# Kernel optimization log

Hardware: AMD Instinct MI355X
Metric: run time of the kernel (lower is better)

The kernel has to match this reference:

```python
import jax, jax.numpy as jnp
import numpy as np

# Production-scale graph dims (see shape_source)
N = 50000      # nodes
E = 800000     # edges (avg degree 16)
C_IN = 128     # input feature dim
H = 96         # hidden (per species: prey X and predator Y)
C_OUT = 40     # num_classes
L = 5          # LVConv layers
DT = 0.05      # integration step


def setup_inputs() -> dict:
    key = jax.random.key(0)
    ks = jax.random.split(key, 14)
    x = jax.random.normal(ks[0], (N, C_IN), jnp.float32)
    edge_index = jax.random.randint(ks[1], (2, E), 0, N, dtype=jnp.int32)
    # lift linears
    Wx = jax.random.normal(ks[2], (C_IN, H), jnp.float32) / np.sqrt(C_IN)
    bx = jnp.zeros((H,), jnp.float32)
    Wy = jax.random.normal(ks[3], (C_IN, H), jnp.float32) / np.sqrt(C_IN)
    by = jnp.zeros((H,), jnp.float32)
    # per-layer Lotka-Volterra coefficients (per-channel), small positive scale
    alpha = 0.1 * jax.random.uniform(ks[4], (L, H), jnp.float32)
    beta  = 0.1 * jax.random.uniform(ks[5], (L, H), jnp.float32)
    gamma = 0.1 * jax.random.uniform(ks[6], (L, H), jnp.float32)
    delta = 0.1 * jax.random.uniform(ks[7], (L, H), jnp.float32)
    # readout on concat([X, Y])
    Wr = jax.random.normal(ks[8], (2 * H, C_OUT), jnp.float32) / np.sqrt(2 * H)
    br = jnp.zeros((C_OUT,), jnp.float32)
    return {"x": x, "edge_index": edge_index, "Wx": Wx, "bx": bx,
            "Wy": Wy, "by": by, "alpha": alpha, "beta": beta,
            "gamma": gamma, "delta": delta, "Wr": Wr, "br": br}


def reference(x, edge_index, Wx, bx, Wy, by, alpha, beta, gamma, delta, Wr, br):
    src, dst = edge_index[0], edge_index[1]
    # in-degree for mean aggregation over incoming edges
    deg = jax.ops.segment_sum(jnp.ones((E,), x.dtype), dst, num_segments=N)
    deg_inv = (1.0 / jnp.maximum(deg, 1.0))[:, None]  # [N,1]

    def mean_agg(v):  # [N,H] -> [N,H] neighbor mean (src -> dst)
        return jax.ops.segment_sum(v[src], dst, num_segments=N) * deg_inv

    # lift to prey (X) and predator (Y) populations
    X = jnp.tanh(x @ Wx + bx)
    Y = jnp.tanh(x @ Wy + by)
    # dropout is identity in eval mode (training=False)
    for l in range(L):
        aggX = mean_agg(X)
        aggY = mean_agg(Y)
        # explicit-Euler Lotka-Volterra dynamics on the graph
        Xn = X + DT * X * (alpha[l] - beta[l] * aggY)
        Yn = Y + DT * Y * (-gamma[l] + delta[l] * aggX)
        X, Y = Xn, Yn
    h = jnp.concatenate([X, Y], axis=-1)  # [N, 2H]
    return h @ Wr + br
```

## Files before the change

### kernel.cpp

```cpp
#include <hip/hip_runtime.h>
#include <hip/hip_bf16.h>
#include <hip/hip_fp16.h>


#define HDIM 96
#define CIN 128
#define COUT 40
#define NLAYER 5
#define DTC 0.05f

#define BK_SHIFT 7
#define BK_SIZE 128
#define EPB 2048
#define BCAP 3072
#define BSTRIDE 4096

typedef float  vfloat2 __attribute__((ext_vector_type(2)));
typedef float  vfloat4 __attribute__((ext_vector_type(4)));
typedef short  vshort8 __attribute__((ext_vector_type(8)));

__device__ __forceinline__ unsigned bf16_rne(float f) {
    unsigned u = __float_as_uint(f);
    return (u + 0x7fffu + ((u >> 16) & 1u)) >> 16;
}

__device__ __forceinline__ unsigned pack_bf16_pair(float xf, float yf) {
    return bf16_rne(xf) | (bf16_rne(yf) << 16);
}

__device__ __forceinline__ unsigned pack_f16_pair(float a, float b) {
    unsigned ha = (unsigned)__half_as_ushort(__float2half_rn(a));
    unsigned hb = (unsigned)__half_as_ushort(__float2half_rn(b));
    return ha | (hb << 16);
}

__device__ __forceinline__ float f16_lo(unsigned u) {
    return __half2float(__ushort_as_half((unsigned short)(u & 0xffffu)));
}
__device__ __forceinline__ float f16_hi(unsigned u) {
    return __half2float(__ushort_as_half((unsigned short)(u >> 16)));
}

__device__ __forceinline__ unsigned pack_fp8_quad(float x0, float y0, float x1, float y1) {
    int lo = __builtin_amdgcn_cvt_pk_fp8_f32(x0, y0, 0, false);
    int full = __builtin_amdgcn_cvt_pk_fp8_f32(x1, y1, lo, true);
    return (unsigned)full;
}

__device__ __forceinline__ float fast_tanh(float x) {
    float e = __expf(2.0f * x);
    return 1.0f - 2.0f * __builtin_amdgcn_rcpf(e + 1.0f);
}


__global__ __launch_bounds__(256) void wprep_kernel(
    const float* __restrict__ Wx, const float* __restrict__ bx,
    const float* __restrict__ Wy, const float* __restrict__ by,
    unsigned short* __restrict__ WcT, float* __restrict__ bc,
    int* __restrict__ gcur, int NB,
    unsigned* __restrict__ F0, unsigned* __restrict__ F1, int N) {
    int t = blockIdx.x * blockDim.x + threadIdx.x;
    if (t < NB) gcur[t] = 0;
    if (t < 192 * 128) {
        int cc = t >> 7;
        int k = t & 127;
        int h = cc >> 1;
        float w = (cc & 1) ? Wy[k * HDIM + h] : Wx[k * HDIM + h];
        WcT[cc * 128 + k] = (unsigned short)bf16_rne(w);
    }
    if (t < 192) {
        int h = t >> 1;
        bc[t] = (t & 1) ? by[h] : bx[h];
    }
    if (blockIdx.x == 0 && threadIdx.x < 48) {
        int plane = threadIdx.x >> 4, d = threadIdx.x & 15;
        size_t o = ((size_t)plane * (N + 1) + N) * 16 + d;
        F0[o] = 0u;
        F1[o] = 0u;
    }
}


__global__ __launch_bounds__(256) void bscatter_kernel(
    const int* __restrict__ src, const int* __restrict__ dst,
    int* __restrict__ gcur, unsigned* __restrict__ packed, int E, int NB) {
    __shared__ int h[512];
    __shared__ int cur[512];
    for (int i = threadIdx.x; i < NB; i += 256) h[i] = 0;
    __syncthreads();
    int base = blockIdx.x * EPB;
    int end = min(E, base + EPB);
    for (int e = base + threadIdx.x; e < end; e += 256)
        atomicAdd(&h[dst[e] >> BK_SHIFT], 1);
    __syncthreads();
    for (int i = threadIdx.x; i < NB; i += 256)
        cur[i] = h[i] ? atomicAdd(&gcur[i], h[i]) : 0;
    __syncthreads();
    for (int e = base + threadIdx.x; e < end; e += 256) {
        int d = dst[e];
        int b = d >> BK_SHIFT;
        int pos = atomicAdd(&cur[b], 1);
        if (pos < BCAP)
            packed[(size_t)b * BCAP + pos] =
                (unsigned)src[e] | ((unsigned)(d & (BK_SIZE - 1)) << 17);
    }
}


__global__ __launch_bounds__(256) void bcsr_kernel(
    const unsigned* __restrict__ packed, const int* __restrict__ gcur,
    uint2* __restrict__ rowinfo, unsigned short* __restrict__ csr, int N, int NB) {
    __shared__ int ldeg[BK_SIZE];
    __shared__ int sscan[BK_SIZE];
    __shared__ int lcur[BK_SIZE];
    int b = blockIdx.x;
    int t = threadIdx.x;
    int cnt = min(gcur[b], BCAP);
    const unsigned* pk = packed + (size_t)b * BCAP;
    int wbase = b * BSTRIDE;
    if (t < BK_SIZE) ldeg[t] = 0;
    __syncthreads();
    for (int e = t; e < cnt; e += 256)
        atomicAdd(&ldeg[(pk[e] >> 17) & (BK_SIZE - 1)], 1);
    __syncthreads();
    int deg = 0, pad = 0;
    if (t < BK_SIZE) {
        deg = ldeg[t];
        pad = (deg + 7) & ~7;
        sscan[t] = pad;
    }
    __syncthreads();
    for (int off = 1; off < BK_SIZE; off <<= 1) {
        int tv = (t < BK_SIZE && t >= off) ? sscan[t - off] : 0;
        __syncthreads();
        if (t < BK_SIZE) sscan[t] += tv;
        __syncthreads();
    }
    int gpos = 0;
    if (t < BK_SIZE) {
        gpos = wbase + sscan[t] - pad;
        lcur[t] = gpos;
        int node = b * BK_SIZE + t;
        if (node < N) {
            rowinfo[node] = make_uint2(
                (unsigned)gpos | ((unsigned)(pad >> 2) << 21),
                __float_as_uint(1.0f / fmaxf((float)deg, 1.0f)));
        }
    }
    __syncthreads();
    for (int e = t; e < cnt; e += 256) {
        unsigned p = pk[e];
        int l = (p >> 17) & (BK_SIZE - 1);
        int pos = atomicAdd(&lcur[l], 1);
        csr[pos] = (unsigned short)(p & 0x1FFFFu);
    }
    __syncthreads();
    if (t < BK_SIZE) {
        for (int p = lcur[t]; p < gpos + pad; p++) csr[p] = (unsigned short)N;
    }
}


#define LW_STRIDE 136
#define TILE_STRIDE 200

__global__ __launch_bounds__(256) void lift_mfma_kernel(
    const float* __restrict__ x, const unsigned short* __restrict__ WcT,
    const float* __restrict__ bc, unsigned* __restrict__ S,
    unsigned* __restrict__ F, int N) {
    __shared__ __align__(16) char smem[192 * LW_STRIDE * 2];
    __shared__ float sBc[192];
    unsigned short* sW = (unsigned short*)smem;
    unsigned short* tile = (unsigned short*)smem;
    int t = threadIdx.x;

    {
        const unsigned* g = (const unsigned*)WcT;
        unsigned* s = (unsigned*)sW;
        for (int i = t; i < 192 * 64; i += 256) {
            int cc = i >> 6;
            int kp = i & 63;
            s[cc * (LW_STRIDE / 2) + kp] = g[i];
        }
    }
    if (t < 192) sBc[t] = bc[t];
    __syncthreads();

    int wv = t >> 6;
    int lane = t & 63;
    int quad = lane >> 4;
    int m = lane & 15;
    int mbase = blockIdx.x * 64 + wv * 16;

    int anode = mbase + m;
    if (anode >= N) anode = N - 1;
    const float* xrow = x + (size_t)anode * CIN;

    vfloat4 acc[12];
#pragma unroll
    for (int i = 0; i < 12; i++) acc[i] = (vfloat4){0.f, 0.f, 0.f, 0.f};

#pragma unroll
    for (int kt = 0; kt < 4; kt++) {
        int k0 = kt * 32 + quad * 8;
        float4 xa = *(const float4*)(xrow + k0);
        float4 xb = *(const float4*)(xrow + k0 + 4);
        uint4 ua;
        ua.x = pack_bf16_pair(xa.x, xa.y);
        ua.y = pack_bf16_pair(xa.z, xa.w);
        ua.z = pack_bf16_pair(xb.x, xb.y);
        ua.w = pack_bf16_pair(xb.z, xb.w);
        vshort8 a = *(vshort8*)&ua;
#pragma unroll
        for (int nt = 0; nt < 12; nt++) {
            vshort8 b = *(const vshort8*)&sW[(nt * 16 + m) * LW_STRIDE + k0];
            acc[nt] = __builtin_amdgcn_mfma_f32_16x16x32_bf16(a, b, acc[nt], 0, 0, 0);
        }
    }

    __syncthreads();
#pragma unroll
    for (int nt = 0; nt < 12; nt++) {
        int ccb = nt * 16 + m;
        float bco = sBc[ccb];
#pragma unroll
        for (int r = 0; r < 4; r++) {
            int nl = wv * 16 + quad * 4 + r;
            float v = fast_tanh(acc[nt][r] + bco);
            tile[nl * TILE_STRIDE + ccb] = __half_as_ushort(__float2half_rn(v));
        }
    }
    __syncthreads();

    int nbase = blockIdx.x * 64;
#pragma unroll
    for (int i = 0; i < 6; i++) {
        int idx = i * 256 + t;
        int nl = idx / 24;
        int pos = idx - nl * 24;
        int node = nbase + nl;
        uint4 u = *(const uint4*)&tile[nl * TILE_STRIDE + pos * 8];
        if (node < N) {
            *(uint4*)(S + (size_t)node * 96 + pos * 4) = u;
            float f0 = f16_lo(u.x), f1 = f16_hi(u.x);
            float f2 = f16_lo(u.y), f3 = f16_hi(u.y);
            float f4 = f16_lo(u.z), f5 = f16_hi(u.z);
            float f6 = f16_lo(u.w), f7 = f16_hi(u.w);
            uint2 fq = make_uint2(pack_fp8_quad(f0, f1, f2, f3),
                                  pack_fp8_quad(f4, f5, f6, f7));
            int plane = pos >> 3;
            int slot = (2 * pos) & 15;
            *(uint2*)(F + ((size_t)plane * (N + 1) + node) * 16 + slot) = fq;
        }
    }
}


__global__ __launch_bounds__(256) void layer_kernel(
    const unsigned* __restrict__ F, unsigned* __restrict__ S,
    unsigned* __restrict__ Fn,
    const uint2* __restrict__ rowinfo, const unsigned short* __restrict__ csr,
    const float* __restrict__ alpha, const float* __restrict__ beta,
    const float* __restrict__ gamma, const float* __restrict__ delta,
    int N, int nblk) {
    int bid = blockIdx.x;
    int plane = bid / nblk;
    int tile = bid - plane * nblk;
    unsigned pstride = (unsigned)(N + 1) * 16u;
    const unsigned* Fp = F + (size_t)plane * pstride;

    int wave = threadIdx.x >> 6;
    int lane = threadIdx.x & 63;
    int li = lane & 7;
    unsigned tli = (unsigned)(2 * li);

    int node = tile * 32 + wave * 8 + (lane >> 3);
    bool nvalid = node < N;
    int nclamp = nvalid ? node : N - 1;
    uint2 ri = rowinfo[nclamp];
    unsigned beg = ri.x & 0x1FFFFFu;
    int cnt = nvalid ? (int)((ri.x >> 21) << 2) : 0;
    float dinv = __uint_as_float(ri.y);

    vfloat2 a0 = {0.f, 0.f}, a1 = {0.f, 0.f}, a2 = {0.f, 0.f}, a3 = {0.f, 0.f};

#define UNP(u)                                                              \
    do {                                                                    \
        a0 += __builtin_amdgcn_cvt_pk_f32_fp8((int)(u).x, false);           \
        a1 += __builtin_amdgcn_cvt_pk_f32_fp8((int)(u).x, true);            \
        a2 += __builtin_amdgcn_cvt_pk_f32_fp8((int)(u).y, false);           \
        a3 += __builtin_amdgcn_cvt_pk_f32_fp8((int)(u).y, true);            \
    } while (0)

    for (int j = 0; j < cnt; j += 8) {
        uint4 w = *(const uint4*)(csr + beg + (unsigned)j);
        unsigned o0 = ((w.x & 0xffffu) << 4) + tli;
        unsigned o1 = ((w.x >> 16) << 4) + tli;
        unsigned o2 = ((w.y & 0xffffu) << 4) + tli;
        unsigned o3 = ((w.y >> 16) << 4) + tli;
        unsigned o4 = ((w.z & 0xffffu) << 4) + tli;
        unsigned o5 = ((w.z >> 16) << 4) + tli;
        unsigned o6 = ((w.w & 0xffffu) << 4) + tli;
        unsigned o7 = ((w.w >> 16) << 4) + tli;
        uint2 u0 = *(const uint2*)(Fp + o0);
        uint2 u1 = *(const uint2*)(Fp + o1);
        uint2 u2 = *(const uint2*)(Fp + o2);
        uint2 u3 = *(const uint2*)(Fp + o3);
        uint2 u4 = *(const uint2*)(Fp + o4);
        uint2 u5 = *(const uint2*)(Fp + o5);
        uint2 u6 = *(const uint2*)(Fp + o6);
        uint2 u7 = *(const uint2*)(Fp + o7);
        UNP(u0); UNP(u1); UNP(u2); UNP(u3);
        UNP(u4); UNP(u5); UNP(u6); UNP(u7);
    }
#undef UNP

    if (!nvalid) return;

    int h0 = plane * 32 + 4 * li;
    float4 av = *(const float4*)(alpha + h0);
    float4 bv = *(const float4*)(beta + h0);
    float4 gv = *(const float4*)(gamma + h0);
    float4 dv = *(const float4*)(delta + h0);
    unsigned* srow = S + (size_t)node * 96 + h0;
    uint4 su = *(const uint4*)srow;

    float x0 = f16_lo(su.x), y0 = f16_hi(su.x);
    float x1 = f16_lo(su.y), y1 = f16_hi(su.y);
    float x2 = f16_lo(su.z), y2 = f16_hi(su.z);
    float x3 = f16_lo(su.w), y3 = f16_hi(su.w);

    float ox0 = x0 + DTC * x0 * (av.x - bv.x * (a0.y * dinv));
    float oy0 = y0 + DTC * y0 * (-gv.x + dv.x * (a0.x * dinv));
    float ox1 = x1 + DTC * x1 * (av.y - bv.y * (a1.y * dinv));
    float oy1 = y1 + DTC * y1 * (-gv.y + dv.y * (a1.x * dinv));
    float ox2 = x2 + DTC * x2 * (av.z - bv.z * (a2.y * dinv));
    float oy2 = y2 + DTC * y2 * (-gv.z + dv.z * (a2.x * dinv));
    float ox3 = x3 + DTC * x3 * (av.w - bv.w * (a3.y * dinv));
    float oy3 = y3 + DTC * y3 * (-gv.w + dv.w * (a3.x * dinv));

    uint4 so;
    so.x = pack_f16_pair(ox0, oy0);
    so.y = pack_f16_pair(ox1, oy1);
    so.z = pack_f16_pair(ox2, oy2);
    so.w = pack_f16_pair(ox3, oy3);
    *(uint4*)srow = so;

    if (Fn) {
        uint2 fo;
        fo.x = pack_fp8_quad(ox0, oy0, ox1, oy1);
        fo.y = pack_fp8_quad(ox2, oy2, ox3, oy3);
        *(uint2*)(Fn + (size_t)plane * pstride + (unsigned)node * 16u + tli) = fo;
    }
}


#define WG_STRIDE 200

__global__ __launch_bounds__(256) void readout_mfma_kernel(
    const unsigned short* __restrict__ sh, const float* __restrict__ Wr,
    const float* __restrict__ br, float* __restrict__ out, int N) {
    __shared__ unsigned short sW[48 * WG_STRIDE];
    __shared__ float sB[48];
    int t = threadIdx.x;

    for (int i = t; i < 48 * 192; i += 256) {
        int n = i / 192;
        int kk = i - n * 192;
        int h = kk >> 1;
        float w = 0.f;
        if (n < COUT) w = (kk & 1) ? Wr[(HDIM + h) * COUT + n] : Wr[h * COUT + n];
        sW[n * WG_STRIDE + kk] = __half_as_ushort(__float2half_rn(w));
    }
    if (t < 48) sB[t] = (t < COUT) ? br[t] : 0.f;
    __syncthreads();

    int wv = t >> 6;
    int lane = t & 63;
    int quad = lane >> 4;
    int m = lane & 15;
    int mbase = blockIdx.x * 64 + wv * 16;

    int anode = mbase + m;
    if (anode >= N) anode = N - 1;
    const unsigned short* arow = sh + (size_t)anode * 192;

    vfloat4 acc0 = {0.f, 0.f, 0.f, 0.f};
    vfloat4 acc1 = {0.f, 0.f, 0.f, 0.f};
    vfloat4 acc2 = {0.f, 0.f, 0.f, 0.f};

#pragma unroll
    for (int kt = 0; kt < 6; kt++) {
        int k0 = kt * 32 + quad * 8;
        vshort8 a = *(const vshort8*)(arow + k0);
        vshort8 b0 = *(const vshort8*)&sW[(0 * 16 + m) * WG_STRIDE + k0];
        vshort8 b1 = *(const vshort8*)&sW[(1 * 16 + m) * WG_STRIDE + k0];
        vshort8 b2 = *(const vshort8*)&sW[(2 * 16 + m) * WG_STRIDE + k0];
        acc0 = __builtin_amdgcn_mfma_f32_16x16x32_f16(a, b0, acc0, 0, 0, 0);
        acc1 = __builtin_amdgcn_mfma_f32_16x16x32_f16(a, b1, acc1, 0, 0, 0);
        acc2 = __builtin_amdgcn_mfma_f32_16x16x32_f16(a, b2, acc2, 0, 0, 0);
    }

    float bo0 = sB[m];
    float bo1 = sB[16 + m];
    float bo2 = (m < 8) ? sB[32 + m] : 0.f;
#pragma unroll
    for (int r = 0; r < 4; r++) {
        int node = mbase + quad * 4 + r;
        if (node < N) {
            float* orow = out + (size_t)node * COUT;
            orow[m] = acc0[r] + bo0;
            orow[16 + m] = acc1[r] + bo1;
            if (m < 8) orow[32 + m] = acc2[r] + bo2;
        }
    }
}


extern "C" void kernel_launch(void* const* d_in, const int* in_sizes, int n_in,
                              void* d_out, int out_size, void* d_ws, size_t ws_size,
                              hipStream_t stream) {
    const float* x     = (const float*)d_in[0];
    const int*   ei    = (const int*)d_in[1];
    const float* Wx    = (const float*)d_in[2];
    const float* bx    = (const float*)d_in[3];
    const float* Wy    = (const float*)d_in[4];
    const float* by    = (const float*)d_in[5];
    const float* alpha = (const float*)d_in[6];
    const float* beta  = (const float*)d_in[7];
    const float* gamma = (const float*)d_in[8];
    const float* delta = (const float*)d_in[9];
    const float* Wr    = (const float*)d_in[10];
    const float* br    = (const float*)d_in[11];

    const int N = in_sizes[0] / CIN;
    const int E = in_sizes[1] / 2;
    const int NB = (N + BK_SIZE - 1) >> BK_SHIFT;
    const int nchunk = (E + EPB - 1) / EPB;
    const int nblk = (N + 31) / 32;

    char* ws = (char*)d_ws;
    size_t off = 0;
    auto alloc = [&](size_t bytes) -> void* {
        off = (off + 255) & ~(size_t)255;
        void* p = ws + off;
        off += bytes;
        return p;
    };
    int* gcur          = (int*)alloc((size_t)NB * sizeof(int));
    unsigned* pckd     = (unsigned*)alloc((size_t)NB * BCAP * sizeof(unsigned));
    uint2* rowinfo     = (uint2*)alloc((size_t)N * sizeof(uint2));
    unsigned short* csr = (unsigned short*)alloc(((size_t)NB * BSTRIDE + 64) * sizeof(unsigned short));
    unsigned* Sa   = (unsigned*)alloc((size_t)N * 96 * sizeof(unsigned));
    unsigned* Fa   = (unsigned*)alloc((size_t)(N + 1) * 48 * sizeof(unsigned));
    unsigned* Fb   = (unsigned*)alloc((size_t)(N + 1) * 48 * sizeof(unsigned));
    unsigned short* WcT = (unsigned short*)alloc((size_t)192 * 128 * sizeof(unsigned short));
    float* bc      = (float*)alloc((size_t)192 * sizeof(float));
    (void)ws_size;

    const int* e_src = ei;
    const int* e_dst = ei + E;

    wprep_kernel<<<(192 * 128 + 255) / 256, 256, 0, stream>>>(
        Wx, bx, Wy, by, WcT, bc, gcur, NB, Fa, Fb, N);

    bscatter_kernel<<<nchunk, 256, 0, stream>>>(e_src, e_dst, gcur, pckd, E, NB);
    bcsr_kernel<<<NB, 256, 0, stream>>>(pckd, gcur, rowinfo, csr, N, NB);

    lift_mfma_kernel<<<(N + 63) / 64, 256, 0, stream>>>(x, WcT, bc, Sa, Fa, N);

    const unsigned* Fc = Fa;
    unsigned* Fnx = Fb;
    for (int l = 0; l < NLAYER; l++) {
        bool last = (l == NLAYER - 1);
        layer_kernel<<<3 * nblk, 256, 0, stream>>>(
            Fc, Sa, last ? (unsigned*)nullptr : Fnx,
            rowinfo, csr,
            alpha + l * HDIM, beta + l * HDIM, gamma + l * HDIM, delta + l * HDIM,
            N, nblk);
        const unsigned* tf = Fc; Fc = Fnx; Fnx = (unsigned*)tf;
    }

    readout_mfma_kernel<<<(N + 63) / 64, 256, 0, stream>>>(
        (const unsigned short*)Sa, Wr, br, (float*)d_out, N);
}
```

Before: 290.2 us.

## Fuse edge scatter and CSR build via grid barrier; stage CSR indices in LDS

Merges the bucket scatter and per-bucket CSR construction into one kernel separated by a software grid-wide barrier, which removes one kernel launch and its gap. The layer kernel now copies each tile's contiguous CSR index span into shared memory and reads neighbor indices from LDS, falling back to global memory when the span is too large. It also unrolls the gather loop by two. The grid barrier assumes all blocks (about 391) are co-resident, which risks deadlock if they are not. The LDS staging adds a block-wide sync and 8KB of shared memory per block.

```diff
diff --git a/kernel.cpp b/kernel.cpp
--- a/kernel.cpp
+++ b/kernel.cpp
@@ -57,7 +57,7 @@
     const float* __restrict__ Wx, const float* __restrict__ bx,
     const float* __restrict__ Wy, const float* __restrict__ by,
     unsigned short* __restrict__ WcT, float* __restrict__ bc,
-    int* __restrict__ gcur, int NB,
+    int* __restrict__ gcur, int NB, unsigned* __restrict__ bar,
     unsigned* __restrict__ F0, unsigned* __restrict__ F1, int N) {
     int t = blockIdx.x * blockDim.x + threadIdx.x;
     if (t < NB) gcur[t] = 0;
@@ -72,49 +72,69 @@
         int h = t >> 1;
         bc[t] = (t & 1) ? by[h] : bx[h];
     }
-    if (blockIdx.x == 0 && threadIdx.x < 48) {
-        int plane = threadIdx.x >> 4, d = threadIdx.x & 15;
-        size_t o = ((size_t)plane * (N + 1) + N) * 16 + d;
-        F0[o] = 0u;
-        F1[o] = 0u;
-    }
-}
-
-
-__global__ __launch_bounds__(256) void bscatter_kernel(
+    if (blockIdx.x == 0) {
+        if (threadIdx.x < 48) {
+            int plane = threadIdx.x >> 4, d = threadIdx.x & 15;
+            size_t o = ((size_t)plane * (N + 1) + N) * 16 + d;
+            F0[o] = 0u;
+            F1[o] = 0u;
+        }
+        if (threadIdx.x == 64) *bar = 0u;
+    }
+}
+
+
+__device__ __forceinline__ void grid_barrier(unsigned* bar, unsigned target) {
+    __syncthreads();
+    if (threadIdx.x == 0) {
+        __threadfence();
+        __hip_atomic_fetch_add(bar, 1u, __ATOMIC_ACQ_REL, __HIP_MEMORY_SCOPE_AGENT);
+        while (__hip_atomic_load(bar, __ATOMIC_ACQUIRE, __HIP_MEMORY_SCOPE_AGENT) < target)
+            __builtin_amdgcn_s_sleep(2);
+    }
+    __syncthreads();
+    __threadfence();
+}
+
+__global__ __launch_bounds__(256) void build_kernel(
     const int* __restrict__ src, const int* __restrict__ dst,
-    int* __restrict__ gcur, unsigned* __restrict__ packed, int E, int NB) {
-    __shared__ int h[512];
-    __shared__ int cur[512];
-    for (int i = threadIdx.x; i < NB; i += 256) h[i] = 0;
-    __syncthreads();
-    int base = blockIdx.x * EPB;
-    int end = min(E, base + EPB);
-    for (int e = base + threadIdx.x; e < end; e += 256)
-        atomicAdd(&h[dst[e] >> BK_SHIFT], 1);
-    __syncthreads();
-    for (int i = threadIdx.x; i < NB; i += 256)
-        cur[i] = h[i] ? atomicAdd(&gcur[i], h[i]) : 0;
-    __syncthreads();
-    for (int e = base + threadIdx.x; e < end; e += 256) {
-        int d = dst[e];
-        int b = d >> BK_SHIFT;
-        int pos = atomicAdd(&cur[b], 1);
-        if (pos < BCAP)
-            packed[(size_t)b * BCAP + pos] =
-                (unsigned)src[e] | ((unsigned)(d & (BK_SIZE - 1)) << 17);
-    }
-}
-
-
-__global__ __launch_bounds__(256) void bcsr_kernel(
-    const unsigned* __restrict__ packed, const int* __restrict__ gcur,
-    uint2* __restrict__ rowinfo, unsigned short* __restrict__ csr, int N, int NB) {
-    __shared__ int ldeg[BK_SIZE];
-    __shared__ int sscan[BK_SIZE];
-    __shared__ int lcur[BK_SIZE];
+    int* __restrict__ gcur, unsigned* __restrict__ packed,
+    uint2* __restrict__ rowinfo, unsigned short* __restrict__ csr,
+    unsigned* __restrict__ bar, int E, int N, int NB) {
+    __shared__ int sh_a[512];
+    __shared__ int sh_b[512];
+    int t = threadIdx.x;
+
+    {
+        int* h = sh_a;
+        int* cur = sh_b;
+        for (int i = t; i < NB; i += 256) h[i] = 0;
+        __syncthreads();
+        int base = blockIdx.x * EPB;
+        int end = min(E, base + EPB);
+        for (int e = base + t; e < end; e += 256)
+            atomicAdd(&h[dst[e] >> BK_SHIFT], 1);
+        __syncthreads();
+        for (int i = t; i < NB; i += 256)
+            cur[i] = h[i] ? atomicAdd(&gcur[i], h[i]) : 0;
+        __syncthreads();
+        for (int e = base + t; e < end; e += 256) {
+            int d = dst[e];
+            int b = d >> BK_SHIFT;
+            int pos = atomicAdd(&cur[b], 1);
+            if (pos < BCAP)
+                packed[(size_t)b * BCAP + pos] =
+                    (unsigned)src[e] | ((unsigned)(d & (BK_SIZE - 1)) << 17);
+        }
+    }
+
+    grid_barrier(bar, gridDim.x);
+
     int b = blockIdx.x;
-    int t = threadIdx.x;
+    if (b >= NB) return;
+    int* ldeg  = sh_a;
+    int* sscan = sh_a + 128;
+    int* lcur  = sh_a + 256;
     int cnt = min(gcur[b], BCAP);
     const unsigned* pk = packed + (size_t)b * BCAP;
     int wbase = b * BSTRIDE;
@@ -256,6 +276,8 @@
 }
 
 
+#define SPAN_CAP 4096
+
 __global__ __launch_bounds__(256) void layer_kernel(
     const unsigned* __restrict__ F, unsigned* __restrict__ S,
     unsigned* __restrict__ Fn,
@@ -263,24 +285,42 @@
     const float* __restrict__ alpha, const float* __restrict__ beta,
     const float* __restrict__ gamma, const float* __restrict__ delta,
     int N, int nblk) {
+    __shared__ __align__(16) unsigned short sidx[SPAN_CAP];
     int bid = blockIdx.x;
     int plane = bid / nblk;
     int tile = bid - plane * nblk;
     unsigned pstride = (unsigned)(N + 1) * 16u;
     const unsigned* Fp = F + (size_t)plane * pstride;
 
-    int wave = threadIdx.x >> 6;
-    int lane = threadIdx.x & 63;
+    int t = threadIdx.x;
+    int wave = t >> 6;
+    int lane = t & 63;
     int li = lane & 7;
     unsigned tli = (unsigned)(2 * li);
 
-    int node = tile * 32 + wave * 8 + (lane >> 3);
+    int n0 = tile * 32;
+    int nlast = min(n0 + 31, N - 1);
+    unsigned ri0x = rowinfo[n0].x;
+    unsigned riLx = rowinfo[nlast].x;
+    unsigned beg0 = ri0x & 0x1FFFFFu;
+    unsigned endL = (riLx & 0x1FFFFFu) + ((riLx >> 21) << 2);
+    int span = (int)(endL - beg0);
+    bool use_lds = (span <= SPAN_CAP);
+    if (use_lds) {
+        const uint4* gs = (const uint4*)(csr + beg0);
+        uint4* ld = (uint4*)sidx;
+        for (int i = t; i < (span >> 3); i += 256) ld[i] = gs[i];
+    }
+
+    int node = n0 + wave * 8 + (lane >> 3);
     bool nvalid = node < N;
     int nclamp = nvalid ? node : N - 1;
     uint2 ri = rowinfo[nclamp];
     unsigned beg = ri.x & 0x1FFFFFu;
     int cnt = nvalid ? (int)((ri.x >> 21) << 2) : 0;
     float dinv = __uint_as_float(ri.y);
+
+    __syncthreads();
 
     vfloat2 a0 = {0.f, 0.f}, a1 = {0.f, 0.f}, a2 = {0.f, 0.f}, a3 = {0.f, 0.f};
 
@@ -292,27 +332,37 @@
         a3 += __builtin_amdgcn_cvt_pk_f32_fp8((int)(u).y, true);            \
     } while (0)
 
-    for (int j = 0; j < cnt; j += 8) {
-        uint4 w = *(const uint4*)(csr + beg + (unsigned)j);
-        unsigned o0 = ((w.x & 0xffffu) << 4) + tli;
-        unsigned o1 = ((w.x >> 16) << 4) + tli;
-        unsigned o2 = ((w.y & 0xffffu) << 4) + tli;
-        unsigned o3 = ((w.y >> 16) << 4) + tli;
-        unsigned o4 = ((w.z & 0xffffu) << 4) + tli;
-        unsigned o5 = ((w.z >> 16) << 4) + tli;
-        unsigned o6 = ((w.w & 0xffffu) << 4) + tli;
-        unsigned o7 = ((w.w >> 16) << 4) + tli;
-        uint2 u0 = *(const uint2*)(Fp + o0);
-        uint2 u1 = *(const uint2*)(Fp + o1);
-        uint2 u2 = *(const uint2*)(Fp + o2);
-        uint2 u3 = *(const uint2*)(Fp + o3);
-        uint2 u4 = *(const uint2*)(Fp + o4);
-        uint2 u5 = *(const uint2*)(Fp + o5);
-        uint2 u6 = *(const uint2*)(Fp + o6);
-        uint2 u7 = *(const uint2*)(Fp + o7);
-        UNP(u0); UNP(u1); UNP(u2); UNP(u3);
-        UNP(u4); UNP(u5); UNP(u6); UNP(u7);
-    }
+#define GBODY(WEXPR)                                                        \
+    _Pragma("unroll 2")                                                     \
+    for (int j = 0; j < cnt; j += 8) {                                      \
+        uint4 w = WEXPR;                                                    \
+        unsigned o0 = ((w.x & 0xffffu) << 4) + tli;                         \
+        unsigned o1 = ((w.x >> 16) << 4) + tli;                             \
+        unsigned o2 = ((w.y & 0xffffu) << 4) + tli;                         \
+        unsigned o3 = ((w.y >> 16) << 4) + tli;                             \
+        unsigned o4 = ((w.z & 0xffffu) << 4) + tli;                         \
+        unsigned o5 = ((w.z >> 16) << 4) + tli;                             \
+        unsigned o6 = ((w.w & 0xffffu) << 4) + tli;                         \
+        unsigned o7 = ((w.w >> 16) << 4) + tli;                             \
+        uint2 u0 = *(const uint2*)(Fp + o0);                                \
+        uint2 u1 = *(const uint2*)(Fp + o1);                                \
+        uint2 u2 = *(const uint2*)(Fp + o2);                                \
+        uint2 u3 = *(const uint2*)(Fp + o3);                                \
+        uint2 u4 = *(const uint2*)(Fp + o4);                                \
+        uint2 u5 = *(const uint2*)(Fp + o5);                                \
+        uint2 u6 = *(const uint2*)(Fp + o6);                                \
+        uint2 u7 = *(const uint2*)(Fp + o7);                                \
+        UNP(u0); UNP(u1); UNP(u2); UNP(u3);                                 \
+        UNP(u4); UNP(u5); UNP(u6); UNP(u7);                                 \
+    }
+
+    if (use_lds) {
+        unsigned lbeg = beg - beg0;
+        GBODY((*(const uint4*)(sidx + lbeg + (unsigned)j)))
+    } else {
+        GBODY((*(const uint4*)(csr + beg + (unsigned)j)))
+    }
+#undef GBODY
 #undef UNP
 
     if (!nvalid) return;
@@ -437,6 +487,7 @@
     const int E = in_sizes[1] / 2;
     const int NB = (N + BK_SIZE - 1) >> BK_SHIFT;
     const int nchunk = (E + EPB - 1) / EPB;
+    const int bgrid = (NB > nchunk) ? NB : nchunk;
     const int nblk = (N + 31) / 32;
 
     char* ws = (char*)d_ws;
@@ -448,6 +499,7 @@
         return p;
     };
     int* gcur          = (int*)alloc((size_t)NB * sizeof(int));
+    unsigned* bar      = (unsigned*)alloc(256);
     unsigned* pckd     = (unsigned*)alloc((size_t)NB * BCAP * sizeof(unsigned));
     uint2* rowinfo     = (uint2*)alloc((size_t)N * sizeof(uint2));
     unsigned short* csr = (unsigned short*)alloc(((size_t)NB * BSTRIDE + 64) * sizeof(unsigned short));
@@ -462,10 +514,10 @@
     const int* e_dst = ei + E;
 
     wprep_kernel<<<(192 * 128 + 255) / 256, 256, 0, stream>>>(
-        Wx, bx, Wy, by, WcT, bc, gcur, NB, Fa, Fb, N);
-
-    bscatter_kernel<<<nchunk, 256, 0, stream>>>(e_src, e_dst, gcur, pckd, E, NB);
-    bcsr_kernel<<<NB, 256, 0, stream>>>(pckd, gcur, rowinfo, csr, N, NB);
+        Wx, bx, Wy, by, WcT, bc, gcur, NB, bar, Fa, Fb, N);
+
+    build_kernel<<<bgrid, 256, 0, stream>>>(
+        e_src, e_dst, gcur, pckd, rowinfo, csr, bar, E, N, NB);
 
     lift_mfma_kernel<<<(N + 63) / 64, 256, 0, stream>>>(x, WcT, bc, Sa, Fa, N);
 
```

Measured after the change: 394.6 us. 1.36x slower.
